# Kernel optimization log

Measured on AMD Instinct MI355X. Metric: run time of the kernel, lower is better.

The kernel has to match this reference:

```python
import jax, jax.numpy as jnp
import numpy as np

B, N, D, S, H, ITERS = 128, 4096, 64, 7, 128, 3
EPS = 1e-8
LN_EPS = 1e-5


def _ln(x, g, b):
    mu = jnp.mean(x, axis=-1, keepdims=True)
    var = jnp.mean(jnp.square(x - mu), axis=-1, keepdims=True)
    return (x - mu) * jax.lax.rsqrt(var + LN_EPS) * g + b


def setup_inputs() -> dict:
    key = jax.random.key(0)
    ks = jax.random.split(key, 20)
    xav = lambda k, shp: jax.random.normal(k, shp, jnp.float32) * (2.0 / sum(shp[-2:])) ** 0.5
    inp = {
        "inputs": jax.random.normal(ks[0], (B, N, D), jnp.float32),
        "noise_bg": jax.random.normal(ks[1], (B, 1, D), jnp.float32),
        "noise_fg": jax.random.normal(ks[2], (B, S - 1, D), jnp.float32),
        "ln_in_g": jnp.ones((D,), jnp.float32), "ln_in_b": jnp.zeros((D,), jnp.float32),
        "ln_slot_g": jnp.ones((D,), jnp.float32), "ln_slot_b": jnp.zeros((D,), jnp.float32),
        "ln_mlp_g": jnp.ones((D,), jnp.float32), "ln_mlp_b": jnp.zeros((D,), jnp.float32),
        "Wq": xav(ks[3], (D, D)), "Wk": xav(ks[4], (D, D)), "Wv": xav(ks[5], (D, D)),
        "W_ih": xav(ks[6], (3 * D, D)), "W_hh": xav(ks[7], (3 * D, D)),
        "b_ih": jnp.zeros((3 * D,), jnp.float32), "b_hh": jnp.zeros((3 * D,), jnp.float32),
        "mlp_w1": xav(ks[8], (H, D)), "mlp_b1": jnp.zeros((H,), jnp.float32),
        "mlp_w2": xav(ks[9], (D, H)), "mlp_b2": jnp.zeros((D,), jnp.float32),
        "slots_bg_mu": xav(ks[10], (1, 1, D)),
        "slots_bg_log_sigma": xav(ks[11], (1, 1, D)),
        "slots_mu": xav(ks[12], (1, 1, D)),
        "slots_log_sigma": xav(ks[13], (1, 1, D)),
    }
    return inp


def _gru(x, h, W_ih, W_hh, b_ih, b_hh):
    # x, h: [M, D]; PyTorch GRUCell math, gate order r, z, n
    gi = x @ W_ih.T + b_ih
    gh = h @ W_hh.T + b_hh
    i_r, i_z, i_n = jnp.split(gi, 3, axis=-1)
    h_r, h_z, h_n = jnp.split(gh, 3, axis=-1)
    r = jax.nn.sigmoid(i_r + h_r)
    z = jax.nn.sigmoid(i_z + h_z)
    n = jnp.tanh(i_n + r * h_n)
    return (1.0 - z) * n + z * h


def reference(inputs, noise_bg, noise_fg, ln_in_g, ln_in_b, ln_slot_g, ln_slot_b,
              ln_mlp_g, ln_mlp_b, Wq, Wk, Wv, W_ih, W_hh, b_ih, b_hh,
              mlp_w1, mlp_b1, mlp_w2, mlp_b2,
              slots_bg_mu, slots_bg_log_sigma, slots_mu, slots_log_sigma):
    x = _ln(inputs, ln_in_g, ln_in_b)          # [B, N, D]
    k = jnp.einsum('bnd,ed->bne', x, Wk)       # [B, N, D]
    v = jnp.einsum('bnd,ed->bne', x, Wv)

    bg = slots_bg_mu + jnp.exp(slots_bg_log_sigma) * noise_bg   # [B, 1, D]
    fg = slots_mu + jnp.exp(slots_log_sigma) * noise_fg          # [B, S-1, D]
    slots = jnp.concatenate([bg, fg], axis=1)                    # [B, S, D]

    scale = D ** (-0.5)
    for _ in range(ITERS):
        slots_prev = slots
        s = _ln(slots, ln_slot_g, ln_slot_b)
        q = jnp.einsum('bsd,ed->bse', s, Wq)                     # [B, S, D]
        logits = scale * jnp.einsum('bnd,bsd->bns', k, q)        # [B, N, S]
        attn = jax.nn.softmax(logits, axis=-1) + EPS             # softmax over slots
        attn = attn / jnp.sum(attn, axis=1, keepdims=True)       # renorm over inputs
        updates = jnp.einsum('bns,bnd->bsd', attn, v)            # [B, S, D]
        h = _gru(updates.reshape(B * S, D), slots_prev.reshape(B * S, D),
                 W_ih, W_hh, b_ih, b_hh).reshape(B, S, D)
        m = _ln(h, ln_mlp_g, ln_mlp_b)
        m = jax.nn.relu(m @ mlp_w1.T + mlp_b1) @ mlp_w2.T + mlp_b2
        slots = h + m
    return slots
```

## Files before the change

kernel.cpp:

```cpp
#include <hip/hip_runtime.h>

#define BB 128
#define NN 4096
#define DD 64
#define SS 7
#define HH 128
#define N_ITERS 3
#define EPS_ATTN 1e-8f
#define LN_EPS 1e-5f

typedef unsigned short ushortT;
using short8  = __attribute__((ext_vector_type(8))) short;
using floatx4 = __attribute__((ext_vector_type(4))) float;

__device__ __forceinline__ float bf2f(int u) {
    return __builtin_bit_cast(float, (unsigned)(u & 0xffff) << 16);
}
__device__ __forceinline__ ushortT f2bf(float f) {
    unsigned x = __builtin_bit_cast(unsigned, f);
    x = x + 0x7fff + ((x >> 16) & 1);
    return (ushortT)(x >> 16);
}
__device__ __forceinline__ void wave_stats64(float x, float& mu, float& var) {
    float s1 = x, s2 = x * x;
#pragma unroll
    for (int off = 32; off > 0; off >>= 1) {
        s1 += __shfl_xor(s1, off);
        s2 += __shfl_xor(s2, off);
    }
    mu  = s1 * (1.f / 64.f);
    var = s2 * (1.f / 64.f) - mu * mu;
}

__global__ void prep_w(const float* __restrict__ Wk, const float* __restrict__ Wv,
                       const float* __restrict__ Wih, const float* __restrict__ Whh,
                       const float* __restrict__ w1, const float* __restrict__ w2,
                       ushortT* __restrict__ Wkv, float* __restrict__ WihT,
                       float* __restrict__ WhhT, float* __restrict__ w1T,
                       float* __restrict__ w2T) {
    int i = blockIdx.x * 256 + threadIdx.x;
    if (i < 8192) {
        float v = (i < 4096) ? Wk[i] : Wv[i - 4096];
        Wkv[i] = f2bf(v);
    } else if (i < 20480) {
        int j = i - 8192; int e = j >> 6, d = j & 63;
        WihT[d * 192 + e] = Wih[j];
    } else if (i < 32768) {
        int j = i - 20480; int e = j >> 6, d = j & 63;
        WhhT[d * 192 + e] = Whh[j];
    } else if (i < 40960) {
        int j = i - 32768; int e = j >> 6, d = j & 63;
        w1T[d * 128 + e] = w1[j];
    } else if (i < 49152) {
        int j = i - 40960; int e = j >> 7, h = j & 127;
        w2T[h * 64 + e] = w2[j];
    }
}

__global__ void prep_slots(const float* __restrict__ nbg, const float* __restrict__ nfg,
                           const float* __restrict__ bgmu, const float* __restrict__ bgls,
                           const float* __restrict__ fmu, const float* __restrict__ fls,
                           float* __restrict__ slots) {
    int i = blockIdx.x * 256 + threadIdx.x;
    int d = i & 63;
    int s = (i >> 6) % 7;
    int b = i / 448;
    float v;
    if (s == 0) v = bgmu[d] + expf(bgls[d]) * nbg[b * 64 + d];
    else        v = fmu[d]  + expf(fls[d])  * nfg[(b * 6 + s - 1) * 64 + d];
    slots[i] = v;
}

__global__ __launch_bounds__(256) void kv_proj(const float* __restrict__ x,
                                               const float* __restrict__ g,
                                               const float* __restrict__ bta,
                                               const ushortT* __restrict__ Wkv,
                                               ushortT* __restrict__ kg,
                                               ushortT* __restrict__ vtg) {
    int t = threadIdx.x, w = t >> 6, lane = t & 63;
    long row0 = (long)blockIdx.x << 6;
    int sub = t & 3, r = t >> 2;
    __shared__ ushortT lds_a[64][72];

    const float* xr = x + (row0 + r) * 64 + sub * 16;
    float4 xa[4];
#pragma unroll
    for (int c = 0; c < 4; ++c) xa[c] = *reinterpret_cast<const float4*>(xr + c * 4);
    float s1 = 0.f, s2 = 0.f;
#pragma unroll
    for (int c = 0; c < 4; ++c) {
        s1 += xa[c].x + xa[c].y + xa[c].z + xa[c].w;
        s2 += xa[c].x * xa[c].x + xa[c].y * xa[c].y +
              xa[c].z * xa[c].z + xa[c].w * xa[c].w;
    }
    s1 += __shfl_xor(s1, 1); s2 += __shfl_xor(s2, 1);
    s1 += __shfl_xor(s1, 2); s2 += __shfl_xor(s2, 2);
    float mu = s1 * (1.f / 64.f);
    float var = s2 * (1.f / 64.f) - mu * mu;
    float rs = rsqrtf(var + LN_EPS);
    unsigned un[8];
#pragma unroll
    for (int c = 0; c < 4; ++c) {
        float4 g4 = *reinterpret_cast<const float4*>(g + sub * 16 + c * 4);
        float4 b4 = *reinterpret_cast<const float4*>(bta + sub * 16 + c * 4);
        float n0 = (xa[c].x - mu) * rs * g4.x + b4.x;
        float n1 = (xa[c].y - mu) * rs * g4.y + b4.y;
        float n2 = (xa[c].z - mu) * rs * g4.z + b4.z;
        float n3 = (xa[c].w - mu) * rs * g4.w + b4.w;
        un[c * 2]     = (unsigned)f2bf(n0) | ((unsigned)f2bf(n1) << 16);
        un[c * 2 + 1] = (unsigned)f2bf(n2) | ((unsigned)f2bf(n3) << 16);
    }
    *reinterpret_cast<uint4*>(&lds_a[r][sub * 16]) =
        make_uint4(un[0], un[1], un[2], un[3]);
    *reinterpret_cast<uint4*>(&lds_a[r][sub * 16 + 8]) =
        make_uint4(un[4], un[5], un[6], un[7]);

    int m = lane & 15, qd = lane >> 4;
    short8 bk[4][2];
#pragma unroll
    for (int tt = 0; tt < 4; ++tt)
#pragma unroll
        for (int c = 0; c < 2; ++c)
            bk[tt][c] = *reinterpret_cast<const short8*>(
                Wkv + (tt * 16 + m) * 64 + c * 32 + qd * 8);
    __syncthreads();

    short8 af[2];
#pragma unroll
    for (int c = 0; c < 2; ++c)
        af[c] = *reinterpret_cast<const short8*>(&lds_a[w * 16 + m][c * 32 + qd * 8]);

    floatx4 ak[4];
#pragma unroll
    for (int tt = 0; tt < 4; ++tt) ak[tt] = (floatx4){0.f, 0.f, 0.f, 0.f};
#pragma unroll
    for (int tt = 0; tt < 4; ++tt)
#pragma unroll
        for (int c = 0; c < 2; ++c)
            ak[tt] = __builtin_amdgcn_mfma_f32_16x16x32_bf16(bk[tt][c], af[c],
                                                             ak[tt], 0, 0, 0);
    short8 bv[4][2];
#pragma unroll
    for (int tt = 0; tt < 4; ++tt)
#pragma unroll
        for (int c = 0; c < 2; ++c)
            bv[tt][c] = *reinterpret_cast<const short8*>(
                Wkv + ((tt + 4) * 16 + m) * 64 + c * 32 + qd * 8);
    floatx4 av[4];
#pragma unroll
    for (int tt = 0; tt < 4; ++tt) av[tt] = (floatx4){0.f, 0.f, 0.f, 0.f};
#pragma unroll
    for (int tt = 0; tt < 4; ++tt)
#pragma unroll
        for (int c = 0; c < 2; ++c)
            av[tt] = __builtin_amdgcn_mfma_f32_16x16x32_bf16(af[c], bv[tt][c],
                                                             av[tt], 0, 0, 0);
    long Rk = row0 + w * 16 + m;
#pragma unroll
    for (int tt = 0; tt < 4; ++tt) {
        uint2 u;
        u.x = (unsigned)f2bf(ak[tt][0]) | ((unsigned)f2bf(ak[tt][1]) << 16);
        u.y = (unsigned)f2bf(ak[tt][2]) | ((unsigned)f2bf(ak[tt][3]) << 16);
        *reinterpret_cast<uint2*>(kg + (Rk << 6) + tt * 16 + qd * 4) = u;
    }
    long vchunk = ((long)(blockIdx.x >> 1)) << 13;
    int rv = (int)(row0 & 127) + w * 16 + qd * 4;
#pragma unroll
    for (int tt = 0; tt < 4; ++tt) {
        int d = tt * 16 + m;
        uint2 u;
        u.x = (unsigned)f2bf(av[tt][0]) | ((unsigned)f2bf(av[tt][1]) << 16);
        u.y = (unsigned)f2bf(av[tt][2]) | ((unsigned)f2bf(av[tt][3]) << 16);
        *reinterpret_cast<uint2*>(vtg + vchunk + d * 128 + rv) = u;
    }
}

__global__ __launch_bounds__(448) void slots_q(const float* __restrict__ slots,
                                               const float* __restrict__ Wq,
                                               const float* __restrict__ g,
                                               const float* __restrict__ bta,
                                               float* __restrict__ qbuf) {
    int b = blockIdx.x, t = threadIdx.x, s = t >> 6, lane = t & 63;
    __shared__ float WqT[64 * 65];
    __shared__ float xn[7][64];
    for (int i = t; i < 4096; i += 448)
        WqT[(i & 63) * 65 + (i >> 6)] = Wq[i];
    float xv = slots[(b * 7 + s) * 64 + lane];
    float mu, var;
    wave_stats64(xv, mu, var);
    xn[s][lane] = (xv - mu) * rsqrtf(var + LN_EPS) * g[lane] + bta[lane];
    __syncthreads();
    float acc = 0.f;
#pragma unroll 8
    for (int d = 0; d < 64; ++d) acc += xn[s][d] * WqT[d * 65 + lane];
    qbuf[(b * 7 + s) * 64 + lane] = acc * 0.125f;
}

__global__ __launch_bounds__(256) void attn_kernel(const ushortT* __restrict__ kg,
                                                   const ushortT* __restrict__ vtg,
                                                   const float* __restrict__ qbuf,
                                                   float* __restrict__ num_p,
                                                   float* __restrict__ den_p) {
    int t = threadIdx.x;
    int ck = blockIdx.x;
    int b = ck >> 5;
    long base = (long)ck << 7;
    __shared__ float   q_lds[7][68];
    __shared__ ushortT p_lds[16][136];
    __shared__ float   den_w[4][8];
    int w = t >> 6, lane = t & 63, m = lane & 15, qd = lane >> 4;
    int sub = t & 3, rr = t >> 2;

    short8 kf[2][2];
#pragma unroll
    for (int p = 0; p < 2; ++p) {
        const short8* kp = reinterpret_cast<const short8*>(
            kg + ((base + p * 64 + rr) << 6) + (sub << 4));
        kf[p][0] = kp[0];
        kf[p][1] = kp[1];
    }
    const ushortT* vb = vtg + ((long)ck << 13) + (long)(w * 16 + m) * 128;
    short8 bf[4];
#pragma unroll
    for (int ks = 0; ks < 4; ++ks)
        bf[ks] = *reinterpret_cast<const short8*>(vb + ks * 32 + qd * 8);
    for (int i = t; i < 448; i += 256) q_lds[i >> 6][i & 63] = qbuf[b * 448 + i];
    __syncthreads();

    float dreg0 = 0.f, dreg1 = 0.f;
    int s0 = sub * 2;
#pragma unroll
    for (int p = 0; p < 2; ++p) {
        int row = p * 64 + rr;
        float kx[16];
#pragma unroll
        for (int j = 0; j < 8; ++j) {
            kx[j]     = bf2f(kf[p][0][j]);
            kx[8 + j] = bf2f(kf[p][1][j]);
        }
        float lg[7];
#pragma unroll
        for (int s = 0; s < 7; ++s) {
            const float4* qp = reinterpret_cast<const float4*>(&q_lds[s][sub << 4]);
            float acc = 0.f;
#pragma unroll
            for (int c = 0; c < 4; ++c) {
                float4 qv = qp[c];
                acc += kx[c * 4 + 0] * qv.x + kx[c * 4 + 1] * qv.y +
                       kx[c * 4 + 2] * qv.z + kx[c * 4 + 3] * qv.w;
            }
            lg[s] = acc;
        }
#pragma unroll
        for (int s = 0; s < 7; ++s) {
            lg[s] += __shfl_xor(lg[s], 1);
            lg[s] += __shfl_xor(lg[s], 2);
        }
        float mx = lg[0];
#pragma unroll
        for (int s = 1; s < 7; ++s) mx = fmaxf(mx, lg[s]);
        float sum = 0.f, ps[7];
#pragma unroll
        for (int s = 0; s < 7; ++s) { ps[s] = __expf(lg[s] - mx); sum += ps[s]; }
        float inv = 1.f / sum;
        float p0 = 0.f, p1 = 0.f;
#pragma unroll
        for (int s = 0; s < 7; ++s) {
            float pv = ps[s] * inv + EPS_ATTN;
            if (s == s0)     p0 = pv;
            if (s == s0 + 1) p1 = pv;
        }
        ushortT pb0 = f2bf(p0);
        p_lds[s0][row] = pb0;
        dreg0 += bf2f(pb0);
        if (sub < 3) {
            ushortT pb1 = f2bf(p1);
            p_lds[s0 + 1][row] = pb1;
            dreg1 += bf2f(pb1);
        }
    }
#pragma unroll
    for (int off = 4; off < 64; off <<= 1) {
        dreg0 += __shfl_xor(dreg0, off);
        dreg1 += __shfl_xor(dreg1, off);
    }
    if (lane < 4) {
        den_w[w][2 * lane] = dreg0;
        if (lane < 3) den_w[w][2 * lane + 1] = dreg1;
    }
    __syncthreads();

    floatx4 acc = (floatx4){0.f, 0.f, 0.f, 0.f};
#pragma unroll
    for (int ks = 0; ks < 4; ++ks) {
        short8 af = *reinterpret_cast<const short8*>(&p_lds[m][ks * 32 + qd * 8]);
        acc = __builtin_amdgcn_mfma_f32_16x16x32_bf16(af, bf[ks], acc, 0, 0, 0);
    }
#pragma unroll
    for (int r = 0; r < 4; ++r) {
        int s = qd * 4 + r;
        if (s < 7) num_p[((long)ck * 7 + s) * 64 + w * 16 + m] = acc[r];
    }
    if (t < 7) den_p[ck * 8 + t] = den_w[0][t] + den_w[1][t] + den_w[2][t] + den_w[3][t];
}

__global__ __launch_bounds__(192) void slot_update(
    const float* __restrict__ num_p, const float* __restrict__ den_p,
    float* __restrict__ slots,
    const float* __restrict__ WihT, const float* __restrict__ WhhT,
    const float* __restrict__ bih, const float* __restrict__ bhh,
    const float* __restrict__ lng, const float* __restrict__ lnb,
    const float* __restrict__ w1T, const float* __restrict__ b1,
    const float* __restrict__ w2T, const float* __restrict__ b2,
    float* __restrict__ outp, int write_out) {
    int bs = blockIdx.x, t = threadIdx.x;
    int b = bs / 7, s = bs % 7;
    __shared__ float upd[64], hprev[64], gi[192], gh[192], hbuf[64], mn[64], m1[128];
    if (t < 64) {
        float nsum = 0.f, dsum = 0.f;
#pragma unroll 4
        for (int c = 0; c < 32; ++c) {
            nsum += num_p[((long)(b * 32 + c) * 7 + s) * 64 + t];
            dsum += den_p[(b * 32 + c) * 8 + s];
        }
        upd[t]   = nsum / dsum;
        hprev[t] = slots[bs * 64 + t];
    }
    __syncthreads();
    {
        float a = bih[t], h = bhh[t];
#pragma unroll 8
        for (int d = 0; d < 64; ++d) {
            a += upd[d] * WihT[d * 192 + t];
            h += hprev[d] * WhhT[d * 192 + t];
        }
        gi[t] = a; gh[t] = h;
    }
    __syncthreads();
    if (t < 64) {
        float r = 1.f / (1.f + __expf(-(gi[t] + gh[t])));
        float z = 1.f / (1.f + __expf(-(gi[64 + t] + gh[64 + t])));
        float n = tanhf(gi[128 + t] + r * gh[128 + t]);
        float h = (1.f - z) * n + z * hprev[t];
        hbuf[t] = h;
        float mu, var;
        wave_stats64(h, mu, var);
        mn[t] = (h - mu) * rsqrtf(var + LN_EPS) * lng[t] + lnb[t];
    }
    __syncthreads();
    if (t < 128) {
        float a = b1[t];
#pragma unroll 8
        for (int d = 0; d < 64; ++d) a += mn[d] * w1T[d * 128 + t];
        m1[t] = fmaxf(a, 0.f);
    }
    __syncthreads();
    if (t < 64) {
        float a = b2[t];
#pragma unroll 8
        for (int h2 = 0; h2 < 128; ++h2) a += m1[h2] * w2T[h2 * 64 + t];
        float res = hbuf[t] + a;
        slots[bs * 64 + t] = res;
        if (write_out) outp[bs * 64 + t] = res;
    }
}

extern "C" void kernel_launch(void* const* d_in, const int* in_sizes, int n_in,
                              void* d_out, int out_size, void* d_ws, size_t ws_size,
                              hipStream_t stream) {
    const float* inputs    = (const float*)d_in[0];
    const float* noise_bg  = (const float*)d_in[1];
    const float* noise_fg  = (const float*)d_in[2];
    const float* ln_in_g   = (const float*)d_in[3];
    const float* ln_in_b   = (const float*)d_in[4];
    const float* ln_slot_g = (const float*)d_in[5];
    const float* ln_slot_b = (const float*)d_in[6];
    const float* ln_mlp_g  = (const float*)d_in[7];
    const float* ln_mlp_b  = (const float*)d_in[8];
    const float* Wq        = (const float*)d_in[9];
    const float* Wk        = (const float*)d_in[10];
    const float* Wv        = (const float*)d_in[11];
    const float* W_ih      = (const float*)d_in[12];
    const float* W_hh      = (const float*)d_in[13];
    const float* b_ih      = (const float*)d_in[14];
    const float* b_hh      = (const float*)d_in[15];
    const float* mlp_w1    = (const float*)d_in[16];
    const float* mlp_b1    = (const float*)d_in[17];
    const float* mlp_w2    = (const float*)d_in[18];
    const float* mlp_b2    = (const float*)d_in[19];
    const float* sbg_mu    = (const float*)d_in[20];
    const float* sbg_ls    = (const float*)d_in[21];
    const float* s_mu      = (const float*)d_in[22];
    const float* s_ls      = (const float*)d_in[23];

    char* ws = (char*)d_ws;
    size_t off = 0;
    auto alloc = [&](size_t bytes) {
        void* p = ws + off;
        off += (bytes + 255) & ~(size_t)255;
        return p;
    };
    ushortT* kg    = (ushortT*)alloc((size_t)BB * NN * 64 * 2);
    ushortT* vtg   = (ushortT*)alloc((size_t)BB * NN * 64 * 2);
    ushortT* Wkv   = (ushortT*)alloc(8192 * 2);
    float* slots   = (float*)alloc(57344 * 4);
    float* qbuf    = (float*)alloc(57344 * 4);
    float* num_p   = (float*)alloc((size_t)4096 * 7 * 64 * 4);
    float* den_p   = (float*)alloc(4096 * 8 * 4);
    float* WihT    = (float*)alloc(12288 * 4);
    float* WhhT    = (float*)alloc(12288 * 4);
    float* w1T     = (float*)alloc(8192 * 4);
    float* w2T     = (float*)alloc(8192 * 4);
    if (off > ws_size) return;

    prep_w<<<192, 256, 0, stream>>>(Wk, Wv, W_ih, W_hh, mlp_w1, mlp_w2,
                                    Wkv, WihT, WhhT, w1T, w2T);
    prep_slots<<<224, 256, 0, stream>>>(noise_bg, noise_fg, sbg_mu, sbg_ls,
                                        s_mu, s_ls, slots);
    kv_proj<<<8192, 256, 0, stream>>>(inputs, ln_in_g, ln_in_b, Wkv, kg, vtg);
    for (int it = 0; it < N_ITERS; ++it) {
        slots_q<<<128, 448, 0, stream>>>(slots, Wq, ln_slot_g, ln_slot_b, qbuf);
        attn_kernel<<<4096, 256, 0, stream>>>(kg, vtg, qbuf, num_p, den_p);
        slot_update<<<896, 192, 0, stream>>>(num_p, den_p, slots, WihT, WhhT,
                                             b_ih, b_hh, ln_mlp_g, ln_mlp_b,
                                             w1T, mlp_b1, w2T, mlp_b2,
                                             (float*)d_out,
                                             (it == N_ITERS - 1) ? 1 : 0);
    }
}
```

Measured before the change: 429.3 us.

## Pre-swizzle K/V and weight layouts for MFMA fragments and fuse slot update with Q projection

```diff
diff --git a/kernel.cpp b/kernel.cpp
--- a/kernel.cpp
+++ b/kernel.cpp
@@ -35,13 +35,18 @@
 __global__ void prep_w(const float* __restrict__ Wk, const float* __restrict__ Wv,
                        const float* __restrict__ Wih, const float* __restrict__ Whh,
                        const float* __restrict__ w1, const float* __restrict__ w2,
-                       ushortT* __restrict__ Wkv, float* __restrict__ WihT,
+                       ushortT* __restrict__ Wkvf, float* __restrict__ WihT,
                        float* __restrict__ WhhT, float* __restrict__ w1T,
                        float* __restrict__ w2T) {
     int i = blockIdx.x * 256 + threadIdx.x;
     if (i < 8192) {
-        float v = (i < 4096) ? Wk[i] : Wv[i - 4096];
-        Wkv[i] = f2bf(v);
+        int c2 = i >> 9, lane = (i >> 3) & 63, j = i & 7;
+        int tile = c2 >> 1, cc = c2 & 1;
+        int qd = lane >> 4, m = lane & 15;
+        int row = tile * 16 + m;
+        int col = cc * 32 + qd * 8 + j;
+        float v = (row < 64) ? Wk[row * 64 + col] : Wv[(row - 64) * 64 + col];
+        Wkvf[i] = f2bf(v);
     } else if (i < 20480) {
         int j = i - 8192; int e = j >> 6, d = j & 63;
         WihT[d * 192 + e] = Wih[j];
@@ -57,24 +62,10 @@
     }
 }
 
-__global__ void prep_slots(const float* __restrict__ nbg, const float* __restrict__ nfg,
-                           const float* __restrict__ bgmu, const float* __restrict__ bgls,
-                           const float* __restrict__ fmu, const float* __restrict__ fls,
-                           float* __restrict__ slots) {
-    int i = blockIdx.x * 256 + threadIdx.x;
-    int d = i & 63;
-    int s = (i >> 6) % 7;
-    int b = i / 448;
-    float v;
-    if (s == 0) v = bgmu[d] + expf(bgls[d]) * nbg[b * 64 + d];
-    else        v = fmu[d]  + expf(fls[d])  * nfg[(b * 6 + s - 1) * 64 + d];
-    slots[i] = v;
-}
-
 __global__ __launch_bounds__(256) void kv_proj(const float* __restrict__ x,
                                                const float* __restrict__ g,
                                                const float* __restrict__ bta,
-                                               const ushortT* __restrict__ Wkv,
+                                               const ushortT* __restrict__ Wkvf,
                                                ushortT* __restrict__ kg,
                                                ushortT* __restrict__ vtg) {
     int t = threadIdx.x, w = t >> 6, lane = t & 63;
@@ -122,7 +113,7 @@
 #pragma unroll
         for (int c = 0; c < 2; ++c)
             bk[tt][c] = *reinterpret_cast<const short8*>(
-                Wkv + (tt * 16 + m) * 64 + c * 32 + qd * 8);
+                Wkvf + (tt * 2 + c) * 512 + lane * 8);
     __syncthreads();
 
     short8 af[2];
@@ -139,61 +130,42 @@
         for (int c = 0; c < 2; ++c)
             ak[tt] = __builtin_amdgcn_mfma_f32_16x16x32_bf16(bk[tt][c], af[c],
                                                              ak[tt], 0, 0, 0);
-    short8 bv[4][2];
-#pragma unroll
-    for (int tt = 0; tt < 4; ++tt)
-#pragma unroll
-        for (int c = 0; c < 2; ++c)
-            bv[tt][c] = *reinterpret_cast<const short8*>(
-                Wkv + ((tt + 4) * 16 + m) * 64 + c * 32 + qd * 8);
-    floatx4 av[4];
-#pragma unroll
-    for (int tt = 0; tt < 4; ++tt) av[tt] = (floatx4){0.f, 0.f, 0.f, 0.f};
-#pragma unroll
-    for (int tt = 0; tt < 4; ++tt)
-#pragma unroll
-        for (int c = 0; c < 2; ++c)
-            av[tt] = __builtin_amdgcn_mfma_f32_16x16x32_bf16(af[c], bv[tt][c],
-                                                             av[tt], 0, 0, 0);
-    long Rk = row0 + w * 16 + m;
+    long kbase = ((long)blockIdx.x << 12) + w * 1024 + lane * 4;
 #pragma unroll
     for (int tt = 0; tt < 4; ++tt) {
         uint2 u;
         u.x = (unsigned)f2bf(ak[tt][0]) | ((unsigned)f2bf(ak[tt][1]) << 16);
         u.y = (unsigned)f2bf(ak[tt][2]) | ((unsigned)f2bf(ak[tt][3]) << 16);
-        *reinterpret_cast<uint2*>(kg + (Rk << 6) + tt * 16 + qd * 4) = u;
-    }
-    long vchunk = ((long)(blockIdx.x >> 1)) << 13;
-    int rv = (int)(row0 & 127) + w * 16 + qd * 4;
+        *reinterpret_cast<uint2*>(kg + kbase + tt * 256) = u;
+    }
+
+    short8 bv[4][2];
+#pragma unroll
+    for (int tt = 0; tt < 4; ++tt)
+#pragma unroll
+        for (int c = 0; c < 2; ++c)
+            bv[tt][c] = *reinterpret_cast<const short8*>(
+                Wkvf + ((tt + 4) * 2 + c) * 512 + lane * 8);
+    floatx4 av[4];
+#pragma unroll
+    for (int tt = 0; tt < 4; ++tt) av[tt] = (floatx4){0.f, 0.f, 0.f, 0.f};
+#pragma unroll
+    for (int tt = 0; tt < 4; ++tt)
+#pragma unroll
+        for (int c = 0; c < 2; ++c)
+            av[tt] = __builtin_amdgcn_mfma_f32_16x16x32_bf16(af[c], bv[tt][c],
+                                                             av[tt], 0, 0, 0);
+    int ks  = (((int)(row0 & 127)) + w * 16) >> 5;
+    int qd2 = (w * 2 + (qd >> 1)) & 3;
+    long vbase = (((long)blockIdx.x >> 1) << 13) + ks * 512 + qd2 * 128 + m * 8 +
+                 (qd & 1) * 4;
 #pragma unroll
     for (int tt = 0; tt < 4; ++tt) {
-        int d = tt * 16 + m;
         uint2 u;
         u.x = (unsigned)f2bf(av[tt][0]) | ((unsigned)f2bf(av[tt][1]) << 16);
         u.y = (unsigned)f2bf(av[tt][2]) | ((unsigned)f2bf(av[tt][3]) << 16);
-        *reinterpret_cast<uint2*>(vtg + vchunk + d * 128 + rv) = u;
-    }
-}
-
-__global__ __launch_bounds__(448) void slots_q(const float* __restrict__ slots,
-                                               const float* __restrict__ Wq,
-                                               const float* __restrict__ g,
-                                               const float* __restrict__ bta,
-                                               float* __restrict__ qbuf) {
-    int b = blockIdx.x, t = threadIdx.x, s = t >> 6, lane = t & 63;
-    __shared__ float WqT[64 * 65];
-    __shared__ float xn[7][64];
-    for (int i = t; i < 4096; i += 448)
-        WqT[(i & 63) * 65 + (i >> 6)] = Wq[i];
-    float xv = slots[(b * 7 + s) * 64 + lane];
-    float mu, var;
-    wave_stats64(xv, mu, var);
-    xn[s][lane] = (xv - mu) * rsqrtf(var + LN_EPS) * g[lane] + bta[lane];
-    __syncthreads();
-    float acc = 0.f;
-#pragma unroll 8
-    for (int d = 0; d < 64; ++d) acc += xn[s][d] * WqT[d * 65 + lane];
-    qbuf[(b * 7 + s) * 64 + lane] = acc * 0.125f;
+        *reinterpret_cast<uint2*>(vtg + vbase + tt * 2048) = u;
+    }
 }
 
 __global__ __launch_bounds__(256) void attn_kernel(const ushortT* __restrict__ kg,
@@ -204,26 +176,26 @@
     int t = threadIdx.x;
     int ck = blockIdx.x;
     int b = ck >> 5;
-    long base = (long)ck << 7;
     __shared__ float   q_lds[7][68];
     __shared__ ushortT p_lds[16][136];
     __shared__ float   den_w[4][8];
     int w = t >> 6, lane = t & 63, m = lane & 15, qd = lane >> 4;
     int sub = t & 3, rr = t >> 2;
 
-    short8 kf[2][2];
+    uint2 kf[2][4];
 #pragma unroll
     for (int p = 0; p < 2; ++p) {
-        const short8* kp = reinterpret_cast<const short8*>(
-            kg + ((base + p * 64 + rr) << 6) + (sub << 4));
-        kf[p][0] = kp[0];
-        kf[p][1] = kp[1];
-    }
-    const ushortT* vb = vtg + ((long)ck << 13) + (long)(w * 16 + m) * 128;
+        const ushortT* kp = kg + ((long)(ck * 2 + p) << 12) + w * 1024 +
+                            sub * 256 + (lane >> 2) * 4;
+#pragma unroll
+        for (int dq = 0; dq < 4; ++dq)
+            kf[p][dq] = *reinterpret_cast<const uint2*>(kp + dq * 64);
+    }
+    const ushortT* vb = vtg + ((long)ck << 13) + w * 2048 + lane * 8;
     short8 bf[4];
 #pragma unroll
     for (int ks = 0; ks < 4; ++ks)
-        bf[ks] = *reinterpret_cast<const short8*>(vb + ks * 32 + qd * 8);
+        bf[ks] = *reinterpret_cast<const short8*>(vb + ks * 512);
     for (int i = t; i < 448; i += 256) q_lds[i >> 6][i & 63] = qbuf[b * 448 + i];
     __syncthreads();
 
@@ -234,9 +206,11 @@
         int row = p * 64 + rr;
         float kx[16];
 #pragma unroll
-        for (int j = 0; j < 8; ++j) {
-            kx[j]     = bf2f(kf[p][0][j]);
-            kx[8 + j] = bf2f(kf[p][1][j]);
+        for (int dq = 0; dq < 4; ++dq) {
+            kx[dq * 4 + 0] = bf2f(kf[p][dq].x);
+            kx[dq * 4 + 1] = bf2f(kf[p][dq].x >> 16);
+            kx[dq * 4 + 2] = bf2f(kf[p][dq].y);
+            kx[dq * 4 + 3] = bf2f(kf[p][dq].y >> 16);
         }
         float lg[7];
 #pragma unroll
@@ -304,65 +278,90 @@
     if (t < 7) den_p[ck * 8 + t] = den_w[0][t] + den_w[1][t] + den_w[2][t] + den_w[3][t];
 }
 
-__global__ __launch_bounds__(192) void slot_update(
+__global__ __launch_bounds__(448) void slot_update_q(
+    int mode,
     const float* __restrict__ num_p, const float* __restrict__ den_p,
     float* __restrict__ slots,
+    const float* __restrict__ nbg, const float* __restrict__ nfg,
+    const float* __restrict__ bgmu, const float* __restrict__ bgls,
+    const float* __restrict__ fmu, const float* __restrict__ fls,
     const float* __restrict__ WihT, const float* __restrict__ WhhT,
     const float* __restrict__ bih, const float* __restrict__ bhh,
     const float* __restrict__ lng, const float* __restrict__ lnb,
     const float* __restrict__ w1T, const float* __restrict__ b1,
     const float* __restrict__ w2T, const float* __restrict__ b2,
-    float* __restrict__ outp, int write_out) {
-    int bs = blockIdx.x, t = threadIdx.x;
-    int b = bs / 7, s = bs % 7;
-    __shared__ float upd[64], hprev[64], gi[192], gh[192], hbuf[64], mn[64], m1[128];
-    if (t < 64) {
+    const float* __restrict__ Wq,
+    const float* __restrict__ sg, const float* __restrict__ sb,
+    float* __restrict__ qbuf, float* __restrict__ outp) {
+    int b = blockIdx.x, t = threadIdx.x, s = t >> 6, l = t & 63;
+    __shared__ float WqT[64 * 65];
+    __shared__ float updL[7][64], hprevL[7][64], mnL[7][64], m1L[7][128], xnL[7][64];
+    if (mode != 2)
+        for (int i = t; i < 4096; i += 448)
+            WqT[(i & 63) * 65 + (i >> 6)] = Wq[i];
+    float res;
+    if (mode == 0) {
+        float v;
+        if (s == 0) v = bgmu[l] + __expf(bgls[l]) * nbg[b * 64 + l];
+        else        v = fmu[l]  + __expf(fls[l])  * nfg[(b * 6 + s - 1) * 64 + l];
+        res = v;
+        __syncthreads();
+    } else {
         float nsum = 0.f, dsum = 0.f;
 #pragma unroll 4
         for (int c = 0; c < 32; ++c) {
-            nsum += num_p[((long)(b * 32 + c) * 7 + s) * 64 + t];
+            nsum += num_p[((long)(b * 32 + c) * 7 + s) * 64 + l];
             dsum += den_p[(b * 32 + c) * 8 + s];
         }
-        upd[t]   = nsum / dsum;
-        hprev[t] = slots[bs * 64 + t];
-    }
-    __syncthreads();
-    {
-        float a = bih[t], h = bhh[t];
+        float hp = slots[(b * 7 + s) * 64 + l];
+        updL[s][l]   = nsum / dsum;
+        hprevL[s][l] = hp;
+        __syncthreads();
+        float gi0 = bih[l], gi1 = bih[64 + l], gi2 = bih[128 + l];
+        float gh0 = bhh[l], gh1 = bhh[64 + l], gh2 = bhh[128 + l];
 #pragma unroll 8
         for (int d = 0; d < 64; ++d) {
-            a += upd[d] * WihT[d * 192 + t];
-            h += hprev[d] * WhhT[d * 192 + t];
-        }
-        gi[t] = a; gh[t] = h;
-    }
-    __syncthreads();
-    if (t < 64) {
-        float r = 1.f / (1.f + __expf(-(gi[t] + gh[t])));
-        float z = 1.f / (1.f + __expf(-(gi[64 + t] + gh[64 + t])));
-        float n = tanhf(gi[128 + t] + r * gh[128 + t]);
-        float h = (1.f - z) * n + z * hprev[t];
-        hbuf[t] = h;
+            float u = updL[s][d], hh = hprevL[s][d];
+            gi0 += u * WihT[d * 192 + l];
+            gi1 += u * WihT[d * 192 + 64 + l];
+            gi2 += u * WihT[d * 192 + 128 + l];
+            gh0 += hh * WhhT[d * 192 + l];
+            gh1 += hh * WhhT[d * 192 + 64 + l];
+            gh2 += hh * WhhT[d * 192 + 128 + l];
+        }
+        float r = 1.f / (1.f + __expf(-(gi0 + gh0)));
+        float z = 1.f / (1.f + __expf(-(gi1 + gh1)));
+        float n = tanhf(gi2 + r * gh2);
+        float h = (1.f - z) * n + z * hp;
         float mu, var;
         wave_stats64(h, mu, var);
-        mn[t] = (h - mu) * rsqrtf(var + LN_EPS) * lng[t] + lnb[t];
-    }
-    __syncthreads();
-    if (t < 128) {
-        float a = b1[t];
+        mnL[s][l] = (h - mu) * rsqrtf(var + LN_EPS) * lng[l] + lnb[l];
+        float a0 = b1[l], a1 = b1[64 + l];
 #pragma unroll 8
-        for (int d = 0; d < 64; ++d) a += mn[d] * w1T[d * 128 + t];
-        m1[t] = fmaxf(a, 0.f);
-    }
-    __syncthreads();
-    if (t < 64) {
-        float a = b2[t];
+        for (int d = 0; d < 64; ++d) {
+            float mv = mnL[s][d];
+            a0 += mv * w1T[d * 128 + l];
+            a1 += mv * w1T[d * 128 + 64 + l];
+        }
+        m1L[s][l]      = fmaxf(a0, 0.f);
+        m1L[s][64 + l] = fmaxf(a1, 0.f);
+        float a2 = b2[l];
 #pragma unroll 8
-        for (int h2 = 0; h2 < 128; ++h2) a += m1[h2] * w2T[h2 * 64 + t];
-        float res = hbuf[t] + a;
-        slots[bs * 64 + t] = res;
-        if (write_out) outp[bs * 64 + t] = res;
-    }
+        for (int h2 = 0; h2 < 128; ++h2) a2 += m1L[s][h2] * w2T[h2 * 64 + l];
+        res = h + a2;
+    }
+    slots[(b * 7 + s) * 64 + l] = res;
+    if (mode == 2) {
+        outp[(b * 7 + s) * 64 + l] = res;
+        return;
+    }
+    float mu, var;
+    wave_stats64(res, mu, var);
+    xnL[s][l] = (res - mu) * rsqrtf(var + LN_EPS) * sg[l] + sb[l];
+    float acc = 0.f;
+#pragma unroll 8
+    for (int d = 0; d < 64; ++d) acc += xnL[s][d] * WqT[d * 65 + l];
+    qbuf[(b * 7 + s) * 64 + l] = acc * 0.125f;
 }
 
 extern "C" void kernel_launch(void* const* d_in, const int* in_sizes, int n_in,
@@ -402,7 +401,7 @@
     };
     ushortT* kg    = (ushortT*)alloc((size_t)BB * NN * 64 * 2);
     ushortT* vtg   = (ushortT*)alloc((size_t)BB * NN * 64 * 2);
-    ushortT* Wkv   = (ushortT*)alloc(8192 * 2);
+    ushortT* Wkvf  = (ushortT*)alloc(8192 * 2);
     float* slots   = (float*)alloc(57344 * 4);
     float* qbuf    = (float*)alloc(57344 * 4);
     float* num_p   = (float*)alloc((size_t)4096 * 7 * 64 * 4);
@@ -414,17 +413,22 @@
     if (off > ws_size) return;
 
     prep_w<<<192, 256, 0, stream>>>(Wk, Wv, W_ih, W_hh, mlp_w1, mlp_w2,
-                                    Wkv, WihT, WhhT, w1T, w2T);
-    prep_slots<<<224, 256, 0, stream>>>(noise_bg, noise_fg, sbg_mu, sbg_ls,
-                                        s_mu, s_ls, slots);
-    kv_proj<<<8192, 256, 0, stream>>>(inputs, ln_in_g, ln_in_b, Wkv, kg, vtg);
+                                    Wkvf, WihT, WhhT, w1T, w2T);
+    slot_update_q<<<128, 448, 0, stream>>>(0, num_p, den_p, slots,
+                                           noise_bg, noise_fg, sbg_mu, sbg_ls,
+                                           s_mu, s_ls, WihT, WhhT, b_ih, b_hh,
+                                           ln_mlp_g, ln_mlp_b, w1T, mlp_b1,
+                                           w2T, mlp_b2, Wq, ln_slot_g, ln_slot_b,
+                                           qbuf, (float*)d_out);
+    kv_proj<<<8192, 256, 0, stream>>>(inputs, ln_in_g, ln_in_b, Wkvf, kg, vtg);
     for (int it = 0; it < N_ITERS; ++it) {
-        slots_q<<<128, 448, 0, stream>>>(slots, Wq, ln_slot_g, ln_slot_b, qbuf);
         attn_kernel<<<4096, 256, 0, stream>>>(kg, vtg, qbuf, num_p, den_p);
-        slot_update<<<896, 192, 0, stream>>>(num_p, den_p, slots, WihT, WhhT,
-                                             b_ih, b_hh, ln_mlp_g, ln_mlp_b,
-                                             w1T, mlp_b1, w2T, mlp_b2,
-                                             (float*)d_out,
-                                             (it == N_ITERS - 1) ? 1 : 0);
-    }
-}
+        slot_update_q<<<128, 448, 0, stream>>>((it == N_ITERS - 1) ? 2 : 1,
+                                               num_p, den_p, slots,
+                                               noise_bg, noise_fg, sbg_mu, sbg_ls,
+                                               s_mu, s_ls, WihT, WhhT, b_ih, b_hh,
+                                               ln_mlp_g, ln_mlp_b, w1T, mlp_b1,
+                                               w2T, mlp_b2, Wq, ln_slot_g, ln_slot_b,
+                                               qbuf, (float*)d_out);
+    }
+}
```

Measured after the change: 399.4 us. 1.07x faster.
